# Optimization experiments

Hardware: AMD Instinct MI355X
Metric: run time of the kernel (lower is better)

Reference implementation:

```python
import jax, jax.numpy as jnp
import numpy as np


def setup_inputs() -> dict:
    key = jax.random.key(0)
    k1, k2 = jax.random.split(key)
    B, V = 128, 128000
    logits = jax.random.normal(k1, (B, V), dtype=jnp.float32) * 2.0
    # temperatures in [0.5, 1.5) to avoid degenerate near-zero division
    temperatures = jax.random.uniform(k2, (B,), dtype=jnp.float32, minval=0.5, maxval=1.5)
    return {"logits": logits, "temperatures": temperatures, "top_k": 50}


def reference(logits, temperatures, top_k):
    # temperature scaling (logits.float().div_(temperatures.unsqueeze(1)))
    scaled = logits.astype(jnp.float32) / temperatures[:, None]  # [B, V]
    # top-k threshold: k-th largest value per row
    kth = jax.lax.top_k(scaled, top_k)[0][:, -1, None]  # [B, 1]
    # mask everything strictly below the k-th value
    masked = jnp.where(scaled < kth, -jnp.inf, scaled)  # [B, V]
    # softmax + multinomial sample == categorical over masked logits
    # (categorical applies a stable log-softmax internally, identical distribution)
    sample_key = jax.random.key(42)
    sample_tokens = jax.random.categorical(sample_key, masked, axis=-1)  # [B] int
    return sample_tokens
```

## Files before the change

### kernel.cpp

```cpp
#include <hip/hip_runtime.h>
#include <stdint.h>

#define SPA   8
#define MAXC  4096

__device__ __forceinline__ void tf2x32(uint32_t c0, uint32_t c1,
                                       uint32_t& o0, uint32_t& o1) {
  const uint32_t ks0 = 0u;
  const uint32_t ks1 = 42u;
  const uint32_t ks2 = 0x1BD11BDAu ^ ks0 ^ ks1;
  uint32_t x0 = c0 + ks0;
  uint32_t x1 = c1 + ks1;
#define TF_ROUND(r) { x0 += x1; x1 = (x1 << (r)) | (x1 >> (32 - (r))); x1 ^= x0; }
  TF_ROUND(13) TF_ROUND(15) TF_ROUND(26) TF_ROUND(6)
  x0 += ks1; x1 += ks2 + 1u;
  TF_ROUND(17) TF_ROUND(29) TF_ROUND(16) TF_ROUND(24)
  x0 += ks2; x1 += ks0 + 2u;
  TF_ROUND(13) TF_ROUND(15) TF_ROUND(26) TF_ROUND(6)
  x0 += ks0; x1 += ks1 + 3u;
  TF_ROUND(17) TF_ROUND(29) TF_ROUND(16) TF_ROUND(24)
  x0 += ks1; x1 += ks2 + 4u;
  TF_ROUND(13) TF_ROUND(15) TF_ROUND(26) TF_ROUND(6)
  x0 += ks2; x1 += ks0 + 5u;
#undef TF_ROUND
  o0 = x0; o1 = x1;
}

__device__ __forceinline__ uint32_t jax_bits(uint32_t i) {
  uint32_t o0, o1;
  tf2x32(0u, i, o0, o1);
  return o0 ^ o1;
}

__device__ __forceinline__ float gumbel_from_bits(uint32_t b) {
  float f = __uint_as_float((b >> 9) | 0x3F800000u) - 1.0f;
  float u = f + 1.17549435e-38f;
  return -logf(-logf(u));
}

__device__ __forceinline__ uint32_t f2key(uint32_t bits) {
  return (bits & 0x80000000u) ? ~bits : (bits | 0x80000000u);
}
__device__ __forceinline__ float key2f(uint32_t key) {
  uint32_t fb = (key & 0x80000000u) ? (key & 0x7FFFFFFFu) : ~key;
  return __uint_as_float(fb);
}

__global__ void zero_kernel(uint32_t* __restrict__ p, int n) {
  int i = blockIdx.x * blockDim.x + threadIdx.x;
  const int stride = gridDim.x * blockDim.x;
  for (; i < n; i += stride) p[i] = 0u;
}

__global__ __launch_bounds__(256) void hist_kernel(
    const float* __restrict__ logits, uint32_t* __restrict__ ghist, int V) {
  const int row = blockIdx.y, slice = blockIdx.x;
  const float* lrow = logits + (size_t)row * V;
  const float4* l4p = (const float4*)lrow;
  const int n4tot = V >> 2;
  const int s4 = slice * n4tot / SPA;
  const int e4 = (slice + 1) * n4tot / SPA;

  __shared__ uint32_t lh[4096];
  for (int i = threadIdx.x; i < 4096; i += 256) lh[i] = 0;
  __syncthreads();

  for (int i = s4 + threadIdx.x; i < e4; i += 256) {
    float4 l4 = l4p[i];
    float lv[4] = {l4.x, l4.y, l4.z, l4.w};
#pragma unroll
    for (int j = 0; j < 4; ++j)
      atomicAdd(&lh[f2key(__float_as_uint(lv[j])) >> 20], 1u);
  }
  if (slice == 0) {
    for (int v = (n4tot << 2) + threadIdx.x; v < V; v += 256)
      atomicAdd(&lh[f2key(__float_as_uint(lrow[v])) >> 20], 1u);
  }
  __syncthreads();

  uint32_t* gh = ghist + (size_t)row * 4096;
  for (int b = threadIdx.x; b < 4096; b += 256)
    if (lh[b]) atomicAdd(&gh[b], lh[b]);
}

__global__ __launch_bounds__(256) void selbin_kernel(
    const uint32_t* __restrict__ ghist, const int* __restrict__ topk_p,
    uint32_t* __restrict__ bin12, uint32_t* __restrict__ remk) {
  const int row = blockIdx.x;
  const uint32_t* gh = ghist + (size_t)row * 4096;
  __shared__ uint32_t lh[4096];
  __shared__ uint32_t gsum[64];
  for (int i = threadIdx.x; i < 4096; i += 256) lh[i] = gh[i];
  __syncthreads();
  if (threadIdx.x < 64) {
    uint32_t g = 0;
    for (int j = 0; j < 64; ++j) g += lh[threadIdx.x * 64 + j];
    gsum[threadIdx.x] = g;
  }
  __syncthreads();
  if (threadIdx.x == 0) {
    const uint32_t kk = (uint32_t)(*topk_p);
    uint32_t cum = 0; int g = 63;
    while (g > 0 && cum + gsum[g] < kk) { cum += gsum[g]; --g; }
    int b = g * 64 + 63;
    while (b > g * 64 && cum + lh[b] < kk) { cum += lh[b]; --b; }
    bin12[row] = (uint32_t)b;
    remk[row] = kk - cum;
  }
}

__global__ __launch_bounds__(256) void compact_kernel(
    const float* __restrict__ logits, const uint32_t* __restrict__ bin12,
    uint32_t* __restrict__ candcnt, uint2* __restrict__ cand, int V) {
  const int row = blockIdx.y, slice = blockIdx.x;
  const uint32_t t = bin12[row] << 20;
  const uint32_t lo = (t >= 64u) ? t - 64u : 0u;
  const float* lrow = logits + (size_t)row * V;
  const float4* l4p = (const float4*)lrow;
  const int n4tot = V >> 2;
  const int s4 = slice * n4tot / SPA;
  const int e4 = (slice + 1) * n4tot / SPA;

  for (int i = s4 + threadIdx.x; i < e4; i += 256) {
    float4 l4 = l4p[i];
    float lv[4] = {l4.x, l4.y, l4.z, l4.w};
    const int v0 = i * 4;
#pragma unroll
    for (int j = 0; j < 4; ++j) {
      uint32_t key = f2key(__float_as_uint(lv[j]));
      if (key >= lo) {
        uint32_t p = atomicAdd(&candcnt[row], 1u);
        if (p < MAXC) cand[(size_t)row * MAXC + p] = make_uint2(key, (uint32_t)(v0 + j));
      }
    }
  }
  if (slice == 0) {
    for (int v = (n4tot << 2) + threadIdx.x; v < V; v += 256) {
      uint32_t key = f2key(__float_as_uint(lrow[v]));
      if (key >= lo) {
        uint32_t p = atomicAdd(&candcnt[row], 1u);
        if (p < MAXC) cand[(size_t)row * MAXC + p] = make_uint2(key, (uint32_t)v);
      }
    }
  }
}

__global__ __launch_bounds__(256) void finalize_kernel(
    const uint2* __restrict__ cand, const uint32_t* __restrict__ candcnt,
    const uint32_t* __restrict__ bin12, const uint32_t* __restrict__ remk,
    const float* __restrict__ temps, int* __restrict__ out, int V) {
  const int row = blockIdx.x;
  const uint32_t n = min(candcnt[row], (uint32_t)MAXC);
  const uint2* cr = cand + (size_t)row * MAXC;
  const uint32_t b12 = bin12[row];

  __shared__ uint32_t lh[4096];
  __shared__ uint32_t gsum[64];
  __shared__ uint32_t s_sel, s_rem;
  __shared__ float s_kth;

  for (int i = threadIdx.x; i < 4096; i += 256) lh[i] = 0;
  __syncthreads();
  for (uint32_t i = threadIdx.x; i < n; i += 256) {
    uint32_t k = cr[i].x;
    if ((k >> 20) == b12) atomicAdd(&lh[(k >> 8) & 0xFFFu], 1u);
  }
  __syncthreads();
  if (threadIdx.x < 64) {
    uint32_t g = 0;
    for (int j = 0; j < 64; ++j) g += lh[threadIdx.x * 64 + j];
    gsum[threadIdx.x] = g;
  }
  __syncthreads();
  if (threadIdx.x == 0) {
    uint32_t kk = remk[row], cum = 0; int g = 63;
    while (g > 0 && cum + gsum[g] < kk) { cum += gsum[g]; --g; }
    int b = g * 64 + 63;
    while (b > g * 64 && cum + lh[b] < kk) { cum += lh[b]; --b; }
    s_sel = (uint32_t)b;
    s_rem = kk - cum;
  }
  __syncthreads();
  const uint32_t sel12 = s_sel;
  const uint32_t kk2 = s_rem;
  __syncthreads();

  for (int i = threadIdx.x; i < 256; i += 256) lh[i] = 0;
  __syncthreads();
  const uint32_t pre24 = (b12 << 12) | sel12;
  for (uint32_t i = threadIdx.x; i < n; i += 256) {
    uint32_t k = cr[i].x;
    if ((k >> 8) == pre24) atomicAdd(&lh[k & 0xFFu], 1u);
  }
  __syncthreads();
  if (threadIdx.x == 0) {
    uint32_t cum = 0; int b = 255;
    while (b > 0 && cum + lh[b] < kk2) { cum += lh[b]; --b; }
    uint32_t kthkey = (b12 << 20) | (sel12 << 8) | (uint32_t)b;
    s_kth = key2f(kthkey) / temps[row];
  }
  __syncthreads();

  const float temp = temps[row];
  const float kth = s_kth;
  const uint32_t rowBase = (uint32_t)(row * V);
  float best = -INFINITY;
  int bestIdx = 0x7FFFFFFF;
  for (uint32_t i = threadIdx.x; i < n; i += 256) {
    uint2 c = cr[i];
    float s = key2f(c.x) / temp;
    if (s < kth) continue;
    float g = gumbel_from_bits(jax_bits(rowBase + c.y));
    float val = s + g;
    int idx = (int)c.y;
    if (val > best || (val == best && idx < bestIdx)) { best = val; bestIdx = idx; }
  }

#pragma unroll
  for (int off = 32; off > 0; off >>= 1) {
    float ov = __shfl_down(best, off, 64);
    int oi = __shfl_down(bestIdx, off, 64);
    if (ov > best || (ov == best && oi < bestIdx)) { best = ov; bestIdx = oi; }
  }
  __shared__ float swv[4];
  __shared__ int swi[4];
  const int wid = threadIdx.x >> 6;
  const int lane = threadIdx.x & 63;
  if (lane == 0) { swv[wid] = best; swi[wid] = bestIdx; }
  __syncthreads();
  if (threadIdx.x == 0) {
    for (int w = 1; w < 4; ++w) {
      if (swv[w] > best || (swv[w] == best && swi[w] < bestIdx)) {
        best = swv[w]; bestIdx = swi[w];
      }
    }
    out[row] = bestIdx;
  }
}

extern "C" void kernel_launch(void* const* d_in, const int* in_sizes, int n_in,
                              void* d_out, int out_size, void* d_ws, size_t ws_size,
                              hipStream_t stream) {
  const float* logits = (const float*)d_in[0];
  const float* temps  = (const float*)d_in[1];
  const int*   topk   = (const int*)d_in[2];
  const int B = in_sizes[1];
  const int V = in_sizes[0] / B;

  uint2*    cand    = (uint2*)d_ws;
  uint32_t* bin12   = (uint32_t*)(cand + (size_t)B * MAXC);
  uint32_t* remk    = bin12 + B;
  uint32_t* candcnt = remk + B;
  uint32_t* ghist   = candcnt + B;

  const int nzero = B + B * 4096;

  zero_kernel<<<2048, 256, 0, stream>>>(candcnt, nzero);
  hist_kernel<<<dim3(SPA, B), 256, 0, stream>>>(logits, ghist, V);
  selbin_kernel<<<B, 256, 0, stream>>>(ghist, topk, bin12, remk);
  compact_kernel<<<dim3(SPA, B), 256, 0, stream>>>(logits, bin12, candcnt, cand, V);
  finalize_kernel<<<B, 256, 0, stream>>>(cand, candcnt, bin12, remk, temps,
                                         (int*)d_out, V);
}
```

Baseline: 153.5 us.

## Fuse sampler pipeline into one cooperative kernel with grid-wide syncs

Replaces the five kernel launches (zero, histogram, bin select, compact, finalize) with a single cooperative kernel that separates the phases with grid.sync. Each block writes its own per-slice histogram instead of using global atomics, which removes the separate zeroing pass; slice-0 blocks then sum the slices. Slices per row drop from 8 to 4 so that 512 blocks can all be resident, as a cooperative launch requires. In exchange the kernel pays for three grid-wide barriers, and slice-0 blocks do the serial select and finalize work while the other blocks of the grid idle.

```diff
diff --git a/kernel.cpp b/kernel.cpp
--- a/kernel.cpp
+++ b/kernel.cpp
@@ -1,7 +1,10 @@
 #include <hip/hip_runtime.h>
+#include <hip/hip_cooperative_groups.h>
 #include <stdint.h>
 
-#define SPA   8
+namespace cg = cooperative_groups;
+
+#define SPA   4
 #define MAXC  4096
 
 __device__ __forceinline__ void tf2x32(uint32_t c0, uint32_t c1,
@@ -46,15 +49,16 @@
   return __uint_as_float(fb);
 }
 
-__global__ void zero_kernel(uint32_t* __restrict__ p, int n) {
-  int i = blockIdx.x * blockDim.x + threadIdx.x;
-  const int stride = gridDim.x * blockDim.x;
-  for (; i < n; i += stride) p[i] = 0u;
-}
-
-__global__ __launch_bounds__(256) void hist_kernel(
-    const float* __restrict__ logits, uint32_t* __restrict__ ghist, int V) {
-  const int row = blockIdx.y, slice = blockIdx.x;
+__global__ __launch_bounds__(256) void fused_sampler(
+    const float* __restrict__ logits, const float* __restrict__ temps,
+    const int* __restrict__ topk_p, uint32_t* __restrict__ ghist,
+    uint32_t* __restrict__ bin12, uint32_t* __restrict__ remk,
+    uint32_t* __restrict__ candcnt, uint2* __restrict__ cand,
+    int* __restrict__ out, int V) {
+  cg::grid_group grid = cg::this_grid();
+  const int bid = blockIdx.x;
+  const int row = bid / SPA, slice = bid % SPA;
+  const int tid = threadIdx.x;
   const float* lrow = logits + (size_t)row * V;
   const float4* l4p = (const float4*)lrow;
   const int n4tot = V >> 2;
@@ -62,179 +66,170 @@
   const int e4 = (slice + 1) * n4tot / SPA;
 
   __shared__ uint32_t lh[4096];
-  for (int i = threadIdx.x; i < 4096; i += 256) lh[i] = 0;
-  __syncthreads();
-
-  for (int i = s4 + threadIdx.x; i < e4; i += 256) {
-    float4 l4 = l4p[i];
-    float lv[4] = {l4.x, l4.y, l4.z, l4.w};
-#pragma unroll
-    for (int j = 0; j < 4; ++j)
-      atomicAdd(&lh[f2key(__float_as_uint(lv[j])) >> 20], 1u);
-  }
-  if (slice == 0) {
-    for (int v = (n4tot << 2) + threadIdx.x; v < V; v += 256)
-      atomicAdd(&lh[f2key(__float_as_uint(lrow[v])) >> 20], 1u);
-  }
-  __syncthreads();
-
-  uint32_t* gh = ghist + (size_t)row * 4096;
-  for (int b = threadIdx.x; b < 4096; b += 256)
-    if (lh[b]) atomicAdd(&gh[b], lh[b]);
-}
-
-__global__ __launch_bounds__(256) void selbin_kernel(
-    const uint32_t* __restrict__ ghist, const int* __restrict__ topk_p,
-    uint32_t* __restrict__ bin12, uint32_t* __restrict__ remk) {
-  const int row = blockIdx.x;
-  const uint32_t* gh = ghist + (size_t)row * 4096;
-  __shared__ uint32_t lh[4096];
-  __shared__ uint32_t gsum[64];
-  for (int i = threadIdx.x; i < 4096; i += 256) lh[i] = gh[i];
-  __syncthreads();
-  if (threadIdx.x < 64) {
-    uint32_t g = 0;
-    for (int j = 0; j < 64; ++j) g += lh[threadIdx.x * 64 + j];
-    gsum[threadIdx.x] = g;
-  }
-  __syncthreads();
-  if (threadIdx.x == 0) {
-    const uint32_t kk = (uint32_t)(*topk_p);
-    uint32_t cum = 0; int g = 63;
-    while (g > 0 && cum + gsum[g] < kk) { cum += gsum[g]; --g; }
-    int b = g * 64 + 63;
-    while (b > g * 64 && cum + lh[b] < kk) { cum += lh[b]; --b; }
-    bin12[row] = (uint32_t)b;
-    remk[row] = kk - cum;
-  }
-}
-
-__global__ __launch_bounds__(256) void compact_kernel(
-    const float* __restrict__ logits, const uint32_t* __restrict__ bin12,
-    uint32_t* __restrict__ candcnt, uint2* __restrict__ cand, int V) {
-  const int row = blockIdx.y, slice = blockIdx.x;
-  const uint32_t t = bin12[row] << 20;
-  const uint32_t lo = (t >= 64u) ? t - 64u : 0u;
-  const float* lrow = logits + (size_t)row * V;
-  const float4* l4p = (const float4*)lrow;
-  const int n4tot = V >> 2;
-  const int s4 = slice * n4tot / SPA;
-  const int e4 = (slice + 1) * n4tot / SPA;
-
-  for (int i = s4 + threadIdx.x; i < e4; i += 256) {
-    float4 l4 = l4p[i];
-    float lv[4] = {l4.x, l4.y, l4.z, l4.w};
-    const int v0 = i * 4;
-#pragma unroll
-    for (int j = 0; j < 4; ++j) {
-      uint32_t key = f2key(__float_as_uint(lv[j]));
-      if (key >= lo) {
-        uint32_t p = atomicAdd(&candcnt[row], 1u);
-        if (p < MAXC) cand[(size_t)row * MAXC + p] = make_uint2(key, (uint32_t)(v0 + j));
-      }
-    }
-  }
-  if (slice == 0) {
-    for (int v = (n4tot << 2) + threadIdx.x; v < V; v += 256) {
-      uint32_t key = f2key(__float_as_uint(lrow[v]));
-      if (key >= lo) {
-        uint32_t p = atomicAdd(&candcnt[row], 1u);
-        if (p < MAXC) cand[(size_t)row * MAXC + p] = make_uint2(key, (uint32_t)v);
-      }
-    }
-  }
-}
-
-__global__ __launch_bounds__(256) void finalize_kernel(
-    const uint2* __restrict__ cand, const uint32_t* __restrict__ candcnt,
-    const uint32_t* __restrict__ bin12, const uint32_t* __restrict__ remk,
-    const float* __restrict__ temps, int* __restrict__ out, int V) {
-  const int row = blockIdx.x;
-  const uint32_t n = min(candcnt[row], (uint32_t)MAXC);
-  const uint2* cr = cand + (size_t)row * MAXC;
-  const uint32_t b12 = bin12[row];
-
-  __shared__ uint32_t lh[4096];
   __shared__ uint32_t gsum[64];
   __shared__ uint32_t s_sel, s_rem;
   __shared__ float s_kth;
-
-  for (int i = threadIdx.x; i < 4096; i += 256) lh[i] = 0;
-  __syncthreads();
-  for (uint32_t i = threadIdx.x; i < n; i += 256) {
-    uint32_t k = cr[i].x;
-    if ((k >> 20) == b12) atomicAdd(&lh[(k >> 8) & 0xFFFu], 1u);
-  }
-  __syncthreads();
-  if (threadIdx.x < 64) {
-    uint32_t g = 0;
-    for (int j = 0; j < 64; ++j) g += lh[threadIdx.x * 64 + j];
-    gsum[threadIdx.x] = g;
-  }
-  __syncthreads();
-  if (threadIdx.x == 0) {
-    uint32_t kk = remk[row], cum = 0; int g = 63;
-    while (g > 0 && cum + gsum[g] < kk) { cum += gsum[g]; --g; }
-    int b = g * 64 + 63;
-    while (b > g * 64 && cum + lh[b] < kk) { cum += lh[b]; --b; }
-    s_sel = (uint32_t)b;
-    s_rem = kk - cum;
-  }
-  __syncthreads();
-  const uint32_t sel12 = s_sel;
-  const uint32_t kk2 = s_rem;
-  __syncthreads();
-
-  for (int i = threadIdx.x; i < 256; i += 256) lh[i] = 0;
-  __syncthreads();
-  const uint32_t pre24 = (b12 << 12) | sel12;
-  for (uint32_t i = threadIdx.x; i < n; i += 256) {
-    uint32_t k = cr[i].x;
-    if ((k >> 8) == pre24) atomicAdd(&lh[k & 0xFFu], 1u);
-  }
-  __syncthreads();
-  if (threadIdx.x == 0) {
-    uint32_t cum = 0; int b = 255;
-    while (b > 0 && cum + lh[b] < kk2) { cum += lh[b]; --b; }
-    uint32_t kthkey = (b12 << 20) | (sel12 << 8) | (uint32_t)b;
-    s_kth = key2f(kthkey) / temps[row];
-  }
-  __syncthreads();
-
-  const float temp = temps[row];
-  const float kth = s_kth;
-  const uint32_t rowBase = (uint32_t)(row * V);
-  float best = -INFINITY;
-  int bestIdx = 0x7FFFFFFF;
-  for (uint32_t i = threadIdx.x; i < n; i += 256) {
-    uint2 c = cr[i];
-    float s = key2f(c.x) / temp;
-    if (s < kth) continue;
-    float g = gumbel_from_bits(jax_bits(rowBase + c.y));
-    float val = s + g;
-    int idx = (int)c.y;
-    if (val > best || (val == best && idx < bestIdx)) { best = val; bestIdx = idx; }
-  }
-
-#pragma unroll
-  for (int off = 32; off > 0; off >>= 1) {
-    float ov = __shfl_down(best, off, 64);
-    int oi = __shfl_down(bestIdx, off, 64);
-    if (ov > best || (ov == best && oi < bestIdx)) { best = ov; bestIdx = oi; }
-  }
   __shared__ float swv[4];
   __shared__ int swi[4];
-  const int wid = threadIdx.x >> 6;
-  const int lane = threadIdx.x & 63;
-  if (lane == 0) { swv[wid] = best; swi[wid] = bestIdx; }
+
+  for (int i = tid; i < 4096; i += 256) lh[i] = 0;
   __syncthreads();
-  if (threadIdx.x == 0) {
-    for (int w = 1; w < 4; ++w) {
-      if (swv[w] > best || (swv[w] == best && swi[w] < bestIdx)) {
-        best = swv[w]; bestIdx = swi[w];
+  for (int i = s4 + tid; i < e4; i += 256) {
+    float4 l4 = l4p[i];
+    float lv[4] = {l4.x, l4.y, l4.z, l4.w};
+#pragma unroll
+    for (int j = 0; j < 4; ++j)
+      atomicAdd(&lh[f2key(__float_as_uint(lv[j])) >> 20], 1u);
+  }
+  if (slice == 0) {
+    for (int v = (n4tot << 2) + tid; v < V; v += 256)
+      atomicAdd(&lh[f2key(__float_as_uint(lrow[v])) >> 20], 1u);
+  }
+  __syncthreads();
+  {
+    uint32_t* gh = ghist + (size_t)bid * 4096;
+    for (int b = tid; b < 4096; b += 256) gh[b] = lh[b];
+  }
+  __threadfence();
+  grid.sync();
+
+  if (slice == 0) {
+    for (int b = tid; b < 4096; b += 256) {
+      uint32_t s = 0;
+#pragma unroll
+      for (int p = 0; p < SPA; ++p)
+        s += ghist[((size_t)(row * SPA + p)) * 4096 + b];
+      lh[b] = s;
+    }
+    __syncthreads();
+    if (tid < 64) {
+      uint32_t g = 0;
+      for (int j = 0; j < 64; ++j) g += lh[tid * 64 + j];
+      gsum[tid] = g;
+    }
+    __syncthreads();
+    if (tid == 0) {
+      const uint32_t kk = (uint32_t)(*topk_p);
+      uint32_t cum = 0; int g = 63;
+      while (g > 0 && cum + gsum[g] < kk) { cum += gsum[g]; --g; }
+      int b = g * 64 + 63;
+      while (b > g * 64 && cum + lh[b] < kk) { cum += lh[b]; --b; }
+      bin12[row] = (uint32_t)b;
+      remk[row] = kk - cum;
+      candcnt[row] = 0u;
+    }
+  }
+  __threadfence();
+  grid.sync();
+
+  {
+    const uint32_t t = bin12[row] << 20;
+    const uint32_t lo = (t >= 64u) ? t - 64u : 0u;
+    for (int i = s4 + tid; i < e4; i += 256) {
+      float4 l4 = l4p[i];
+      float lv[4] = {l4.x, l4.y, l4.z, l4.w};
+      const int v0 = i * 4;
+#pragma unroll
+      for (int j = 0; j < 4; ++j) {
+        uint32_t key = f2key(__float_as_uint(lv[j]));
+        if (key >= lo) {
+          uint32_t p = atomicAdd(&candcnt[row], 1u);
+          if (p < MAXC) cand[(size_t)row * MAXC + p] = make_uint2(key, (uint32_t)(v0 + j));
+        }
       }
     }
-    out[row] = bestIdx;
+    if (slice == 0) {
+      for (int v = (n4tot << 2) + tid; v < V; v += 256) {
+        uint32_t key = f2key(__float_as_uint(lrow[v]));
+        if (key >= lo) {
+          uint32_t p = atomicAdd(&candcnt[row], 1u);
+          if (p < MAXC) cand[(size_t)row * MAXC + p] = make_uint2(key, (uint32_t)v);
+        }
+      }
+    }
+  }
+  __threadfence();
+  grid.sync();
+
+  if (slice == 0) {
+    const uint32_t n = min(candcnt[row], (uint32_t)MAXC);
+    const uint2* cr = cand + (size_t)row * MAXC;
+    const uint32_t b12 = bin12[row];
+
+    for (int i = tid; i < 4096; i += 256) lh[i] = 0;
+    __syncthreads();
+    for (uint32_t i = tid; i < n; i += 256) {
+      uint32_t k = cr[i].x;
+      if ((k >> 20) == b12) atomicAdd(&lh[(k >> 8) & 0xFFFu], 1u);
+    }
+    __syncthreads();
+    if (tid < 64) {
+      uint32_t g = 0;
+      for (int j = 0; j < 64; ++j) g += lh[tid * 64 + j];
+      gsum[tid] = g;
+    }
+    __syncthreads();
+    if (tid == 0) {
+      uint32_t kk = remk[row], cum = 0; int g = 63;
+      while (g > 0 && cum + gsum[g] < kk) { cum += gsum[g]; --g; }
+      int b = g * 64 + 63;
+      while (b > g * 64 && cum + lh[b] < kk) { cum += lh[b]; --b; }
+      s_sel = (uint32_t)b;
+      s_rem = kk - cum;
+    }
+    __syncthreads();
+    const uint32_t sel12 = s_sel;
+    const uint32_t kk2 = s_rem;
+    __syncthreads();
+
+    for (int i = tid; i < 256; i += 256) lh[i] = 0;
+    __syncthreads();
+    const uint32_t pre24 = (b12 << 12) | sel12;
+    for (uint32_t i = tid; i < n; i += 256) {
+      uint32_t k = cr[i].x;
+      if ((k >> 8) == pre24) atomicAdd(&lh[k & 0xFFu], 1u);
+    }
+    __syncthreads();
+    if (tid == 0) {
+      uint32_t cum = 0; int b = 255;
+      while (b > 0 && cum + lh[b] < kk2) { cum += lh[b]; --b; }
+      uint32_t kthkey = (b12 << 20) | (sel12 << 8) | (uint32_t)b;
+      s_kth = key2f(kthkey) / temps[row];
+    }
+    __syncthreads();
+
+    const float temp = temps[row];
+    const float kth = s_kth;
+    const uint32_t rowBase = (uint32_t)(row * V);
+    float best = -INFINITY;
+    int bestIdx = 0x7FFFFFFF;
+    for (uint32_t i = tid; i < n; i += 256) {
+      uint2 c = cr[i];
+      float s = key2f(c.x) / temp;
+      if (s < kth) continue;
+      float g = gumbel_from_bits(jax_bits(rowBase + c.y));
+      float val = s + g;
+      int idx = (int)c.y;
+      if (val > best || (val == best && idx < bestIdx)) { best = val; bestIdx = idx; }
+    }
+#pragma unroll
+    for (int off = 32; off > 0; off >>= 1) {
+      float ov = __shfl_down(best, off, 64);
+      int oi = __shfl_down(bestIdx, off, 64);
+      if (ov > best || (ov == best && oi < bestIdx)) { best = ov; bestIdx = oi; }
+    }
+    const int wid = tid >> 6;
+    const int lane = tid & 63;
+    if (lane == 0) { swv[wid] = best; swi[wid] = bestIdx; }
+    __syncthreads();
+    if (tid == 0) {
+      for (int w = 1; w < 4; ++w) {
+        if (swv[w] > best || (swv[w] == best && swi[w] < bestIdx)) {
+          best = swv[w]; bestIdx = swi[w];
+        }
+      }
+      out[row] = bestIdx;
+    }
   }
 }
 
@@ -246,6 +241,7 @@
   const int*   topk   = (const int*)d_in[2];
   const int B = in_sizes[1];
   const int V = in_sizes[0] / B;
+  int* out = (int*)d_out;
 
   uint2*    cand    = (uint2*)d_ws;
   uint32_t* bin12   = (uint32_t*)(cand + (size_t)B * MAXC);
@@ -253,12 +249,9 @@
   uint32_t* candcnt = remk + B;
   uint32_t* ghist   = candcnt + B;
 
-  const int nzero = B + B * 4096;
-
-  zero_kernel<<<2048, 256, 0, stream>>>(candcnt, nzero);
-  hist_kernel<<<dim3(SPA, B), 256, 0, stream>>>(logits, ghist, V);
-  selbin_kernel<<<B, 256, 0, stream>>>(ghist, topk, bin12, remk);
-  compact_kernel<<<dim3(SPA, B), 256, 0, stream>>>(logits, bin12, candcnt, cand, V);
-  finalize_kernel<<<B, 256, 0, stream>>>(cand, candcnt, bin12, remk, temps,
-                                         (int*)d_out, V);
-}
+  void* args[] = {(void*)&logits, (void*)&temps, (void*)&topk,
+                  (void*)&ghist, (void*)&bin12, (void*)&remk,
+                  (void*)&candcnt, (void*)&cand, (void*)&out, (void*)&V};
+  hipLaunchCooperativeKernel((const void*)fused_sampler,
+                             dim3(B * SPA), dim3(256), args, 0, stream);
+}
```

After: 478.2 us. 211% more time.
